# Kernel tuning notes

Hardware: AMD Instinct MI355X
Metric: run time of the kernel (lower is better)

The kernel has to match this reference:

```python
import jax, jax.numpy as jnp
import numpy as np

B, S, D, DI = 8, 4096, 512, 2048
EPS = 1e-12  # torch F.normalize eps


def _l2norm(x):
    n = jnp.sqrt(jnp.sum(x * x, axis=-1, keepdims=True))
    return x / jnp.maximum(n, EPS)


def setup_inputs() -> dict:
    key = jax.random.key(0)
    ks = jax.random.split(key, 10)
    sd = 1.0 / np.sqrt(D)
    si = 1.0 / np.sqrt(DI)
    return {
        "x": jax.random.normal(ks[0], (B, S, D), jnp.float32),
        "wq": jax.random.uniform(ks[1], (D, DI), jnp.float32, -sd, sd),
        "wk": jax.random.uniform(ks[2], (D, DI), jnp.float32, -sd, sd),
        "wv": jax.random.uniform(ks[3], (D, DI), jnp.float32, -sd, sd),
        "wo": jax.random.uniform(ks[4], (DI, D), jnp.float32, -si, si),
        "w1": jax.random.uniform(ks[5], (D, DI), jnp.float32, -sd, sd),
        "b1": jax.random.uniform(ks[6], (DI,), jnp.float32, -sd, sd),
        "w2": jax.random.uniform(ks[7], (DI, D), jnp.float32, -si, si),
        "b2": jax.random.uniform(ks[8], (D,), jnp.float32, -si, si),
    }


def reference(x, wq, wk, wv, wo, w1, b1, w2, b2):
    # Hydra attention (linear): normalize(q) * sum_s(normalize(k)*v)
    q = _l2norm(jnp.einsum('bsd,de->bse', x, wq))
    k = _l2norm(jnp.einsum('bsd,de->bse', x, wk))
    v = jnp.einsum('bsd,de->bse', x, wv)
    kv = jnp.sum(k * v, axis=-2, keepdims=True)  # [B,1,DI]
    attn = jnp.einsum('bse,ed->bsd', q * kv, wo) + x  # dropout = identity (eval)
    # position-wise FFN with residual
    h = jax.nn.relu(jnp.einsum('bsd,de->bse', attn, w1) + b1)
    out = jnp.einsum('bse,ed->bsd', h, w2) + b2 + attn
    return out
```

## Files before the change

### kernel.cpp

```cpp
#include <hip/hip_runtime.h>
#include <stdint.h>

#define Bb  8
#define Ss  4096
#define Dd  512
#define DIi 2048
#define Mm  (Bb*Ss)

typedef unsigned short u16;
typedef __bf16 bf16x8 __attribute__((ext_vector_type(8)));
typedef float  f32x4  __attribute__((ext_vector_type(4)));

__device__ __forceinline__ float bfu(unsigned int u) {
  return __uint_as_float((u & 0xffffu) << 16);
}
__device__ __forceinline__ u16 f2bu(float f) {
  unsigned int x = __float_as_uint(f);
  return (u16)((x + 0x7fffu + ((x >> 16) & 1u)) >> 16);
}

__device__ __forceinline__ void tr_tile(const float* __restrict__ W, u16* __restrict__ Wt,
                                        int K, int N, int local, int tid) {
  __shared__ float t[32][33];
  const int nx = N / 32;
  const int n0 = (local % nx) * 32, k0 = (local / nx) * 32;
  const int tx = tid & 31, ty = tid >> 5;
#pragma unroll
  for (int i = 0; i < 32; i += 8)
    t[ty + i][tx] = W[(long)(k0 + ty + i) * N + n0 + tx];
  __syncthreads();
#pragma unroll
  for (int i = 0; i < 32; i += 8)
    Wt[(long)(n0 + ty + i) * K + k0 + tx] = f2bu(t[tx][ty + i]);
}

__global__ __launch_bounds__(256) void prep(
    const float* __restrict__ x, u16* __restrict__ xb,
    const float* wv, const float* w1, const float* wo, const float* w2,
    const float* wq, const float* wk,
    u16* wvT, u16* w1T, u16* woT, u16* w2T, u16* wqb, u16* wkb,
    float* __restrict__ zptr) {
  const int bid = blockIdx.x, tid = threadIdx.x;
  if (bid < 256) {
    zptr[bid * 256 + tid] = 0.f;
  } else if (bid < 2304) {
    long i = (long)(bid - 256) * 256 + tid;
    const long n4 = (long)Mm * Dd / 4;
    const long st = 2048L * 256;
    for (; i < n4; i += st) {
      float4 v = ((const float4*)x)[i];
      ushort4 o;
      o.x = f2bu(v.x); o.y = f2bu(v.y); o.z = f2bu(v.z); o.w = f2bu(v.w);
      ((ushort4*)xb)[i] = o;
    }
  } else if (bid < 3328)  tr_tile(wv, wvT, Dd, DIi, bid - 2304, tid);
  else if (bid < 4352)    tr_tile(w1, w1T, Dd, DIi, bid - 3328, tid);
  else if (bid < 5376)    tr_tile(wo, woT, DIi, Dd, bid - 4352, tid);
  else if (bid < 6400)    tr_tile(w2, w2T, DIi, Dd, bid - 5376, tid);
  else if (bid < 7424) {
    long i = (long)(bid - 6400) * 256 + tid;
    float4 v = ((const float4*)wq)[i];
    ushort4 o;
    o.x = f2bu(v.x); o.y = f2bu(v.y); o.z = f2bu(v.z); o.w = f2bu(v.w);
    ((ushort4*)wqb)[i] = o;
  } else {
    long i = (long)(bid - 7424) * 256 + tid;
    float4 v = ((const float4*)wk)[i];
    ushort4 o;
    o.x = f2bu(v.x); o.y = f2bu(v.y); o.z = f2bu(v.z); o.w = f2bu(v.w);
    ((ushort4*)wkb)[i] = o;
  }
}

__global__ __launch_bounds__(256) void build_wob(const u16* __restrict__ woT,
                                                 const float* __restrict__ kv,
                                                 u16* __restrict__ wob) {
  const int b = blockIdx.y;
  long i = (long)blockIdx.x * 256 + threadIdx.x;
  const long tot = (long)Dd * DIi / 8;
  if (i >= tot) return;
  const long e = i * 8;
  const int k = (int)(e & (DIi - 1));
  ushort4 w0 = *(const ushort4*)(woT + e);
  ushort4 w1 = *(const ushort4*)(woT + e + 4);
  const float* kvp = kv + (long)b * DIi + k;
  ushort4 o0, o1;
  o0.x = f2bu(bfu(w0.x) * kvp[0]); o0.y = f2bu(bfu(w0.y) * kvp[1]);
  o0.z = f2bu(bfu(w0.z) * kvp[2]); o0.w = f2bu(bfu(w0.w) * kvp[3]);
  o1.x = f2bu(bfu(w1.x) * kvp[4]); o1.y = f2bu(bfu(w1.y) * kvp[5]);
  o1.z = f2bu(bfu(w1.z) * kvp[6]); o1.w = f2bu(bfu(w1.w) * kvp[7]);
  u16* dst = wob + (long)b * Dd * DIi + e;
  *(ushort4*)dst = o0;
  *(ushort4*)(dst + 4) = o1;
}

__global__ void tr_x(const u16* __restrict__ xb, const float* __restrict__ nksq,
                     u16* __restrict__ xT, u16* __restrict__ xrnT) {
  __shared__ u16 t[32][33];
  __shared__ float rns[32];
  const int b = blockIdx.z;
  const int s0 = blockIdx.y * 32, d0 = blockIdx.x * 32;
  const int tx = threadIdx.x, ty = threadIdx.y;
  const size_t sbase = (size_t)b * Ss + s0;
#pragma unroll
  for (int i = 0; i < 32; i += 8)
    t[ty + i][tx] = xb[(sbase + ty + i) * Dd + d0 + tx];
  if (ty == 0) {
    const float nk = fmaxf(nksq[sbase + tx], 0.f);
    rns[tx] = 1.f / fmaxf(sqrtf(nk), 1e-12f);
  }
  __syncthreads();
  const size_t dbase = (size_t)b * Dd + d0;
#pragma unroll
  for (int i = 0; i < 32; i += 8) {
    const u16 v = t[tx][ty + i];
    const size_t idx = (dbase + ty + i) * Ss + s0 + tx;
    xT[idx] = v;
    xrnT[idx] = f2bu(bfu(v) * rns[tx]);
  }
}

__global__ __launch_bounds__(256) void colsum_kv(const u16* __restrict__ wkb,
                                                 const u16* __restrict__ Tb,
                                                 float* __restrict__ kv) {
  const int b = blockIdx.y;
  const int e0 = blockIdx.x * 1024 + threadIdx.x * 4;
  const u16* wp = wkb + e0;
  const u16* tp = Tb + (size_t)b * Dd * DIi + e0;
  float a0 = 0, a1 = 0, a2 = 0, a3 = 0;
  for (int d = 0; d < Dd; ++d) {
    ushort4 w = *(const ushort4*)wp;
    ushort4 t = *(const ushort4*)tp;
    a0 += bfu(w.x) * bfu(t.x);
    a1 += bfu(w.y) * bfu(t.y);
    a2 += bfu(w.z) * bfu(t.z);
    a3 += bfu(w.w) * bfu(t.w);
    wp += DIi; tp += DIi;
  }
  float* o = kv + (size_t)b * DIi + e0;
  o[0] = a0; o[1] = a1; o[2] = a2; o[3] = a3;
}

#define GLL(src, dst) \
  __builtin_amdgcn_global_load_lds((const __attribute__((address_space(1))) unsigned int*)(src), \
                                   (__attribute__((address_space(3))) unsigned int*)(dst), 16, 0, 0)

enum { G_FFN1 = 2, G_FFN2 = 3 };

template<int MODE>
__global__ __launch_bounds__(512, 2) void gemm8(
    const u16* __restrict__ A, const u16* __restrict__ Bt,
    int N, int K,
    u16* __restrict__ Ybf, float* __restrict__ Yf,
    const u16* __restrict__ resb, const float* __restrict__ bias)
{
  __shared__ u16 lds8[65536];

  const int bx = blockIdx.x;
  const int by = blockIdx.y;
  const int tid  = threadIdx.x;
  const int lane = tid & 63;
  const int wid  = tid >> 6;
  const int wr = wid >> 2, wc = wid & 3;
  const int l15 = lane & 15, lg = lane >> 4;

  const long bm0 = (long)by * 256;
  const long bn0 = (long)bx * 256;
  const int NT = K >> 6;

  const u16* pA = A + bm0 * K;
  const u16* pB = Bt + bn0 * K;

  const int rowT = ((tid >> 6) << 3) | (tid & 7);
  const int cc8  = ((tid >> 3) & 7) * 8;

#define STAGE(PTR, LD, H, TT, BUFU, REGU) do {                                  \
    const u16* s0_ = (PTR) + (size_t)((H) * 128 + rowT) * (LD)                  \
                     + (size_t)(TT) * 64 + cc8;                                 \
    u16* d_ = lds8 + (BUFU) + (REGU) + (H) * 8192 + wid * 512;                  \
    GLL(s0_, d_);                                                               \
    GLL(s0_ + (size_t)64 * (LD), d_ + 4096);                                    \
  } while (0)

  const int aoff = (wr * 16384 + (l15 >> 3) * 1024 + lg * 128 + (l15 & 7) * 16) >> 1;
  const int boff = (32768 + (wc >> 1) * 16384 + (wc & 1) * 8192 +
                    (l15 >> 3) * 1024 + lg * 128 + (l15 & 7) * 16) >> 1;
#define LDA(M_, KS_, BU_) (*(const bf16x8*)(lds8 + (BU_) + aoff + (M_) * 1024 + (KS_) * 256))
#define LDB(N_, KS_, BU_) (*(const bf16x8*)(lds8 + (BU_) + boff + (N_) * 1024 + (KS_) * 256))

  f32x4 acc[8][4] = {};

  STAGE(pA, K, 0, 0, 0, 0);
  STAGE(pA, K, 1, 0, 0, 0);
  STAGE(pB, K, 0, 0, 0, 16384);
  STAGE(pB, K, 1, 0, 0, 16384);
  STAGE(pA, K, 0, 1, 32768, 0);
  asm volatile("s_waitcnt vmcnt(2)" ::: "memory");
  __builtin_amdgcn_s_barrier();

  for (int t = 0; t < NT; ++t) {
    const int bufu = (t & 1) * 32768;
    const int nbuf = bufu ^ 32768;
    bf16x8 aF[4], bF[4];

#pragma unroll
    for (int n = 0; n < 4; ++n) bF[n] = LDB(n, 0, bufu);
#pragma unroll
    for (int m = 0; m < 4; ++m) aF[m] = LDA(m, 0, bufu);
    if (t + 1 < NT) STAGE(pA, K, 1, t + 1, nbuf, 0);
    __builtin_amdgcn_s_barrier();
    __builtin_amdgcn_s_setprio(1);
#pragma unroll
    for (int m = 0; m < 4; ++m)
#pragma unroll
      for (int n = 0; n < 4; ++n)
        acc[m][n] = __builtin_amdgcn_mfma_f32_16x16x32_bf16(aF[m], bF[n], acc[m][n], 0, 0, 0);
    __builtin_amdgcn_s_setprio(0);

#pragma unroll
    for (int m = 0; m < 4; ++m) aF[m] = LDA(4 + m, 0, bufu);
    if (t + 1 < NT) STAGE(pB, K, 0, t + 1, nbuf, 16384);
    __builtin_amdgcn_s_barrier();
    __builtin_amdgcn_s_setprio(1);
#pragma unroll
    for (int m = 0; m < 4; ++m)
#pragma unroll
      for (int n = 0; n < 4; ++n)
        acc[4 + m][n] = __builtin_amdgcn_mfma_f32_16x16x32_bf16(aF[m], bF[n], acc[4 + m][n], 0, 0, 0);
    __builtin_amdgcn_s_setprio(0);

#pragma unroll
    for (int n = 0; n < 4; ++n) bF[n] = LDB(n, 1, bufu);
#pragma unroll
    for (int m = 0; m < 4; ++m) aF[m] = LDA(m, 1, bufu);
    if (t + 1 < NT) STAGE(pB, K, 1, t + 1, nbuf, 16384);
    __builtin_amdgcn_s_barrier();
    __builtin_amdgcn_s_setprio(1);
#pragma unroll
    for (int m = 0; m < 4; ++m)
#pragma unroll
      for (int n = 0; n < 4; ++n)
        acc[m][n] = __builtin_amdgcn_mfma_f32_16x16x32_bf16(aF[m], bF[n], acc[m][n], 0, 0, 0);
    __builtin_amdgcn_s_setprio(0);

#pragma unroll
    for (int m = 0; m < 4; ++m) aF[m] = LDA(4 + m, 1, bufu);
    __builtin_amdgcn_s_barrier();
    __builtin_amdgcn_s_setprio(1);
#pragma unroll
    for (int m = 0; m < 4; ++m)
#pragma unroll
      for (int n = 0; n < 4; ++n)
        acc[4 + m][n] = __builtin_amdgcn_mfma_f32_16x16x32_bf16(aF[m], bF[n], acc[4 + m][n], 0, 0, 0);
    __builtin_amdgcn_s_setprio(0);

    if (t + 1 < NT) {
      __builtin_amdgcn_s_barrier();
      if (t + 2 < NT) {
        STAGE(pA, K, 0, t + 2, bufu, 0);
        asm volatile("s_waitcnt vmcnt(2)" ::: "memory");
      } else {
        asm volatile("s_waitcnt vmcnt(0)" ::: "memory");
      }
      __builtin_amdgcn_s_barrier();
    }
  }

#pragma unroll
  for (int m = 0; m < 8; ++m) {
    const long row0 = bm0 + wr * 128 + m * 16 + lg * 4;
#pragma unroll
    for (int n = 0; n < 4; ++n) {
      const long col = bn0 + wc * 64 + n * 16 + l15;
#pragma unroll
      for (int r = 0; r < 4; ++r) {
        const long idx = (row0 + r) * N + col;
        const float v = acc[m][n][r];
        if constexpr (MODE == G_FFN1) {
          float o = v + bias[col];
          o = o > 0.f ? o : 0.f;
          Ybf[idx] = f2bu(o);
        } else {
          Yf[idx] = v + bias[col] + bfu(resb[idx]);
        }
      }
    }
  }
#undef STAGE
#undef LDA
#undef LDB
}

__global__ __launch_bounds__(256) void mega_small(
    const u16* __restrict__ wqb, const u16* __restrict__ wkb,
    const u16* __restrict__ wob,
    u16* __restrict__ Gt, u16* __restrict__ Gkt, u16* __restrict__ Ut, int zbase)
{
  __shared__ u16 As[4096];
  __shared__ u16 Bs[4096];
  const int K = DIi;
  const int idx = blockIdx.z + zbase;
  const u16* A  = (idx == 1) ? wkb : wqb;
  const u16* Bt = (idx == 0) ? wqb : (idx == 1) ? wkb
                  : wob + (size_t)(idx - 2) * Dd * DIi;
  u16* Ct = (idx == 0) ? Gt : (idx == 1) ? Gkt
            : Ut + (size_t)(idx - 2) * Dd * Dd;

  const int tid = threadIdx.x, lane = tid & 63, w = tid >> 6;
  const int wr = w >> 1, wc = w & 1;
  const int l15 = lane & 15, lg = lane >> 4;
  const long bm0 = (long)blockIdx.y * 128;
  const long bn0 = (long)blockIdx.x * 128;

  const int c0 = tid, c1 = tid + 256;
  const u16* aS0 = A  + (bm0 + (c0 >> 2)) * K + (c0 & 3) * 8;
  const u16* aS1 = A  + (bm0 + (c1 >> 2)) * K + (c1 & 3) * 8;
  const u16* bS0 = Bt + (bn0 + (c0 >> 2)) * K + (c0 & 3) * 8;
  const u16* bS1 = Bt + (bn0 + (c1 >> 2)) * K + (c1 & 3) * 8;
  u16* aD0 = As + w * 512;
  u16* aD1 = As + 2048 + w * 512;
  u16* bD0 = Bs + w * 512;
  u16* bD1 = Bs + 2048 + w * 512;

  f32x4 acc[4][4] = {};

  for (int k0 = 0; k0 < K; k0 += 32) {
    GLL(aS0 + k0, aD0);
    GLL(aS1 + k0, aD1);
    GLL(bS0 + k0, bD0);
    GLL(bS1 + k0, bD1);
    __syncthreads();
    bf16x8 af[4], bfv[4];
#pragma unroll
    for (int m = 0; m < 4; ++m)
      af[m] = *(const bf16x8*)(As + (wr * 64 + m * 16 + l15) * 32 + lg * 8);
#pragma unroll
    for (int n = 0; n < 4; ++n)
      bfv[n] = *(const bf16x8*)(Bs + (wc * 64 + n * 16 + l15) * 32 + lg * 8);
#pragma unroll
    for (int m = 0; m < 4; ++m)
#pragma unroll
      for (int n = 0; n < 4; ++n)
        acc[m][n] = __builtin_amdgcn_mfma_f32_16x16x32_bf16(af[m], bfv[n], acc[m][n], 0, 0, 0);
    __syncthreads();
  }

#pragma unroll
  for (int m = 0; m < 4; ++m) {
    const int row0 = (int)bm0 + wr * 64 + m * 16 + lg * 4;
#pragma unroll
    for (int n = 0; n < 4; ++n) {
      const int col = (int)bn0 + wc * 64 + n * 16 + l15;
      ushort4 o;
      o.x = f2bu(acc[m][n][0]); o.y = f2bu(acc[m][n][1]);
      o.z = f2bu(acc[m][n][2]); o.w = f2bu(acc[m][n][3]);
      *(ushort4*)(Ct + (size_t)col * Dd + row0) = o;
    }
  }
}

template<int MODE>
__global__ __launch_bounds__(256) void mega128b(
    const u16* __restrict__ A0, const u16* __restrict__ Bt0,
    u16* __restrict__ C0, int N, int K)
{
  __shared__ u16 As[4096];
  __shared__ u16 Bs[4096];
  const int z = blockIdx.z;
  const u16* A  = A0 + (size_t)z * (MODE == 0 ? (size_t)Dd * Ss : (size_t)Dd * Dd);
  const u16* Bt = (MODE == 0) ? Bt0 + (size_t)z * Dd * Ss : Bt0;
  u16* C = C0 + (size_t)z * (MODE == 0 ? (size_t)Dd * Dd : (size_t)Dd * DIi);

  const int tid = threadIdx.x, lane = tid & 63, w = tid >> 6;
  const int wr = w >> 1, wc = w & 1;
  const int l15 = lane & 15, lg = lane >> 4;
  const long bm0 = (long)blockIdx.y * 128;
  const long bn0 = (long)blockIdx.x * 128;

  const int c0 = tid, c1 = tid + 256;
  const u16* aS0 = A  + (bm0 + (c0 >> 2)) * K + (c0 & 3) * 8;
  const u16* aS1 = A  + (bm0 + (c1 >> 2)) * K + (c1 & 3) * 8;
  const u16* bS0 = Bt + (bn0 + (c0 >> 2)) * K + (c0 & 3) * 8;
  const u16* bS1 = Bt + (bn0 + (c1 >> 2)) * K + (c1 & 3) * 8;
  u16* aD0 = As + w * 512;
  u16* aD1 = As + 2048 + w * 512;
  u16* bD0 = Bs + w * 512;
  u16* bD1 = Bs + 2048 + w * 512;

  f32x4 acc[4][4] = {};

  for (int k0 = 0; k0 < K; k0 += 32) {
    GLL(aS0 + k0, aD0);
    GLL(aS1 + k0, aD1);
    GLL(bS0 + k0, bD0);
    GLL(bS1 + k0, bD1);
    __syncthreads();
    bf16x8 af[4], bfv[4];
#pragma unroll
    for (int m = 0; m < 4; ++m)
      af[m] = *(const bf16x8*)(As + (wr * 64 + m * 16 + l15) * 32 + lg * 8);
#pragma unroll
    for (int n = 0; n < 4; ++n)
      bfv[n] = *(const bf16x8*)(Bs + (wc * 64 + n * 16 + l15) * 32 + lg * 8);
#pragma unroll
    for (int m = 0; m < 4; ++m)
#pragma unroll
      for (int n = 0; n < 4; ++n)
        acc[m][n] = __builtin_amdgcn_mfma_f32_16x16x32_bf16(af[m], bfv[n], acc[m][n], 0, 0, 0);
    __syncthreads();
  }

#pragma unroll
  for (int m = 0; m < 4; ++m) {
    const long row0 = bm0 + wr * 64 + m * 16 + lg * 4;
#pragma unroll
    for (int n = 0; n < 4; ++n) {
      const long col = bn0 + wc * 64 + n * 16 + l15;
#pragma unroll
      for (int r = 0; r < 4; ++r)
        C[(row0 + r) * N + col] = f2bu(acc[m][n][r]);
    }
  }
}

template<int MODE>
__global__ __launch_bounds__(256) void mega_nx(
    const u16* __restrict__ xb, const u16* __restrict__ Gt, const u16* __restrict__ Gkt,
    const u16* __restrict__ Ut,
    float* __restrict__ nqsq, float* __restrict__ nksq, u16* __restrict__ attnb)
{
  __shared__ u16 As[4096];
  __shared__ u16 Bs[4096];
  __shared__ u16 xs[16384];
  const int K = Dd, N = Dd;

  const int tid = threadIdx.x, lane = tid & 63, w = tid >> 6;
  const int wr = w >> 1, wc = w & 1;
  const int l15 = lane & 15, lg = lane >> 4;
  const bool isK = (MODE == 0) && (blockIdx.y >= Mm / 128);
  const long bm0 = (long)(isK ? blockIdx.y - Mm / 128 : blockIdx.y) * 128;
  const long bn0 = (long)blockIdx.x * 128;
  const int bq = (int)(bm0 >> 12);
  const u16* Bt = (MODE == 0) ? (isK ? Gkt : Gt) : Ut + (size_t)bq * Dd * Dd;
  float* nsq = (MODE == 0) ? (isK ? nksq : nqsq) : nqsq;

  const int c0 = tid, c1 = tid + 256;
  const u16* aS0 = xb + (bm0 + (c0 >> 2)) * K + (c0 & 3) * 8;
  const u16* aS1 = xb + (bm0 + (c1 >> 2)) * K + (c1 & 3) * 8;
  const u16* bS0 = Bt + (bn0 + (c0 >> 2)) * K + (c0 & 3) * 8;
  const u16* bS1 = Bt + (bn0 + (c1 >> 2)) * K + (c1 & 3) * 8;
  u16* aD0 = As + w * 512;
  u16* aD1 = As + 2048 + w * 512;
  u16* bD0 = Bs + w * 512;
  u16* bD1 = Bs + 2048 + w * 512;

  f32x4 acc[4][4] = {};

  for (int k0 = 0; k0 < K; k0 += 32) {
    GLL(aS0 + k0, aD0);
    GLL(aS1 + k0, aD1);
    GLL(bS0 + k0, bD0);
    GLL(bS1 + k0, bD1);
    __syncthreads();
    bf16x8 af[4], bfv[4];
#pragma unroll
    for (int m = 0; m < 4; ++m)
      af[m] = *(const bf16x8*)(As + (wr * 64 + m * 16 + l15) * 32 + lg * 8);
#pragma unroll
    for (int n = 0; n < 4; ++n)
      bfv[n] = *(const bf16x8*)(Bs + (wc * 64 + n * 16 + l15) * 32 + lg * 8);
#pragma unroll
    for (int m = 0; m < 4; ++m)
#pragma unroll
      for (int n = 0; n < 4; ++n)
        acc[m][n] = __builtin_amdgcn_mfma_f32_16x16x32_bf16(af[m], bfv[n], acc[m][n], 0, 0, 0);
    __syncthreads();
  }

#pragma unroll
  for (int i = 0; i < 8; ++i) {
    const int c = i * 256 + tid;
    const int rowL = c >> 4;
    const int srcslot = (c & 15) ^ (rowL & 15);
    const u16* src = xb + (size_t)(bm0 + rowL) * Dd + bn0 + srcslot * 8;
    GLL(src, xs + i * 2048 + w * 512);
  }
  asm volatile("s_waitcnt vmcnt(0)" ::: "memory");
  __builtin_amdgcn_s_barrier();

#define XV(RL, CL) bfu(xs[(RL) * 128 + ((((CL) >> 3) ^ ((RL) & 15)) << 3) + ((CL) & 7)])

  if constexpr (MODE == 0) {
    float sk[16];
#pragma unroll
    for (int i = 0; i < 16; ++i) sk[i] = 0.f;
#pragma unroll
    for (int m = 0; m < 4; ++m) {
#pragma unroll
      for (int n = 0; n < 4; ++n) {
        const int colL = wc * 64 + n * 16 + l15;
#pragma unroll
        for (int r = 0; r < 4; ++r) {
          const int rowL = wr * 64 + m * 16 + lg * 4 + r;
          sk[m * 4 + r] += acc[m][n][r] * XV(rowL, colL);
        }
      }
    }
#pragma unroll
    for (int i = 0; i < 16; ++i) {
#pragma unroll
      for (int off = 1; off < 16; off <<= 1)
        sk[i] += __shfl_xor(sk[i], off, 64);
    }
    if (l15 == 0) {
#pragma unroll
      for (int m = 0; m < 4; ++m)
#pragma unroll
        for (int r = 0; r < 4; ++r)
          atomicAdd(&nsq[bm0 + wr * 64 + m * 16 + lg * 4 + r], sk[m * 4 + r]);
    }
  } else {
#pragma unroll
    for (int m = 0; m < 4; ++m) {
      const long row0 = bm0 + wr * 64 + m * 16 + lg * 4;
      float rq[4];
#pragma unroll
      for (int r = 0; r < 4; ++r)
        rq[r] = 1.f / fmaxf(sqrtf(fmaxf(nqsq[row0 + r], 0.f)), 1e-12f);
#pragma unroll
      for (int n = 0; n < 4; ++n) {
        const int colL = wc * 64 + n * 16 + l15;
#pragma unroll
        for (int r = 0; r < 4; ++r) {
          const int rowL = wr * 64 + m * 16 + lg * 4 + r;
          attnb[(row0 + r) * N + bn0 + colL] = f2bu(acc[m][n][r] * rq[r] + XV(rowL, colL));
        }
      }
    }
  }
#undef XV
}

extern "C" void kernel_launch(void* const* d_in, const int* in_sizes, int n_in,
                              void* d_out, int out_size, void* d_ws, size_t ws_size,
                              hipStream_t stream) {
  const float* x  = (const float*)d_in[0];
  const float* wq = (const float*)d_in[1];
  const float* wk = (const float*)d_in[2];
  const float* wv = (const float*)d_in[3];
  const float* wo = (const float*)d_in[4];
  const float* w1 = (const float*)d_in[5];
  const float* b1 = (const float*)d_in[6];
  const float* w2 = (const float*)d_in[7];
  const float* b2 = (const float*)d_in[8];
  float* out = (float*)d_out;

  char* p = (char*)d_ws;
  auto take = [&](size_t bytes) {
    char* r = p; p += (bytes + 255) & ~(size_t)255; return r;
  };
  u16*   xb    = (u16*)take((size_t)Mm * Dd * 2);
  u16*   wvT   = (u16*)take((size_t)DIi * Dd * 2);
  u16*   w1T   = (u16*)take((size_t)DIi * Dd * 2);
  u16*   woT   = (u16*)take((size_t)Dd * DIi * 2);
  u16*   w2T   = (u16*)take((size_t)Dd * DIi * 2);
  u16*   wqb   = (u16*)take((size_t)Dd * DIi * 2);
  u16*   wkb   = (u16*)take((size_t)Dd * DIi * 2);
  u16*   Gt    = (u16*)take((size_t)Dd * Dd * 2);
  u16*   Gkt   = (u16*)take((size_t)Dd * Dd * 2);
  u16*   Ut    = (u16*)take((size_t)Bb * Dd * Dd * 2);
  u16*   buf1  = (u16*)take((size_t)Mm * DIi * 2);
  u16*   attnb = (u16*)take((size_t)Mm * Dd * 2);
  float* nksq  = (float*)take((size_t)Mm * 4);
  float* nqsq  = (float*)take((size_t)Mm * 4);
  float* kvp   = (float*)take((size_t)Bb * DIi * 4);
  u16* xT   = buf1;
  u16* xrnT = buf1 + (size_t)Mm * Dd;
  u16* Tb   = buf1 + 2 * (size_t)Mm * Dd;
  u16* Cb   = buf1 + 2 * (size_t)Mm * Dd + (size_t)Bb * Dd * DIi;
  u16* wob  = buf1 + 2 * (size_t)Mm * Dd + (size_t)Bb * Dd * DIi
                   + (size_t)Bb * Dd * Dd;
  (void)in_sizes; (void)n_in; (void)out_size; (void)ws_size;

  prep<<<8448, 256, 0, stream>>>(x, xb, wv, w1, wo, w2, wq, wk,
                                 wvT, w1T, woT, w2T, wqb, wkb, nksq);

  mega_small<<<dim3(4, 4, 2), 256, 0, stream>>>(wqb, wkb, nullptr, Gt, Gkt, Ut, 0);

  mega_nx<0><<<dim3(4, 2 * Mm / 128), 256, 0, stream>>>(
      xb, Gt, Gkt, nullptr, nqsq, nksq, nullptr);

  tr_x<<<dim3(Dd / 32, Ss / 32, Bb), dim3(32, 8), 0, stream>>>(xb, nksq, xT, xrnT);

  mega128b<0><<<dim3(4, 4, Bb), 256, 0, stream>>>(xrnT, xT, Cb, Dd, Ss);

  mega128b<1><<<dim3(16, 4, Bb), 256, 0, stream>>>(Cb, wvT, Tb, DIi, Dd);

  colsum_kv<<<dim3(2, Bb), 256, 0, stream>>>(wkb, Tb, kvp);

  build_wob<<<dim3(512, Bb), 256, 0, stream>>>(woT, kvp, wob);

  mega_small<<<dim3(4, 4, 8), 256, 0, stream>>>(wqb, wkb, wob, Gt, Gkt, Ut, 2);

  mega_nx<1><<<dim3(4, Mm / 128), 256, 0, stream>>>(
      xb, nullptr, nullptr, Ut, nqsq, nullptr, attnb);

  gemm8<G_FFN1><<<dim3(DIi / 256, Mm / 256), 512, 0, stream>>>(
      attnb, w1T, DIi, Dd, buf1, nullptr, nullptr, b1);

  gemm8<G_FFN2><<<dim3(Dd / 256, Mm / 256), 512, 0, stream>>>(
      buf1, w2T, Dd, DIi, nullptr, out, attnb, b2);
}
```

Baseline: 552.7 us.

## Raise parallelism of the Cb GEMM and split-reduce the kv column sum

The batched xrnT·xT GEMM now uses 64x64 tiles, giving 512 blocks instead of 128, so the long K=4096 reduction is spread over many more CUs. The column-sum kernel that produces kv is split along the D dimension into 8 chunks, and the partial sums are combined with atomicAdd. The prep kernel zeroes a larger region so the kv buffer starts at zero before the atomics. The trade-offs are less data reuse per tile, more global traffic, and atomic contention plus non-deterministic summation order for kv.

```diff
diff --git a/kernel.cpp b/kernel.cpp
--- a/kernel.cpp
+++ b/kernel.cpp
@@ -41,10 +41,10 @@
     u16* wvT, u16* w1T, u16* woT, u16* w2T, u16* wqb, u16* wkb,
     float* __restrict__ zptr) {
   const int bid = blockIdx.x, tid = threadIdx.x;
-  if (bid < 256) {
+  if (bid < 320) {
     zptr[bid * 256 + tid] = 0.f;
-  } else if (bid < 2304) {
-    long i = (long)(bid - 256) * 256 + tid;
+  } else if (bid < 2368) {
+    long i = (long)(bid - 320) * 256 + tid;
     const long n4 = (long)Mm * Dd / 4;
     const long st = 2048L * 256;
     for (; i < n4; i += st) {
@@ -53,18 +53,18 @@
       o.x = f2bu(v.x); o.y = f2bu(v.y); o.z = f2bu(v.z); o.w = f2bu(v.w);
       ((ushort4*)xb)[i] = o;
     }
-  } else if (bid < 3328)  tr_tile(wv, wvT, Dd, DIi, bid - 2304, tid);
-  else if (bid < 4352)    tr_tile(w1, w1T, Dd, DIi, bid - 3328, tid);
-  else if (bid < 5376)    tr_tile(wo, woT, DIi, Dd, bid - 4352, tid);
-  else if (bid < 6400)    tr_tile(w2, w2T, DIi, Dd, bid - 5376, tid);
-  else if (bid < 7424) {
-    long i = (long)(bid - 6400) * 256 + tid;
+  } else if (bid < 3392)  tr_tile(wv, wvT, Dd, DIi, bid - 2368, tid);
+  else if (bid < 4416)    tr_tile(w1, w1T, Dd, DIi, bid - 3392, tid);
+  else if (bid < 5440)    tr_tile(wo, woT, DIi, Dd, bid - 4416, tid);
+  else if (bid < 6464)    tr_tile(w2, w2T, DIi, Dd, bid - 5440, tid);
+  else if (bid < 7488) {
+    long i = (long)(bid - 6464) * 256 + tid;
     float4 v = ((const float4*)wq)[i];
     ushort4 o;
     o.x = f2bu(v.x); o.y = f2bu(v.y); o.z = f2bu(v.z); o.w = f2bu(v.w);
     ((ushort4*)wqb)[i] = o;
   } else {
-    long i = (long)(bid - 7424) * 256 + tid;
+    long i = (long)(bid - 7488) * 256 + tid;
     float4 v = ((const float4*)wk)[i];
     ushort4 o;
     o.x = f2bu(v.x); o.y = f2bu(v.y); o.z = f2bu(v.z); o.w = f2bu(v.w);
@@ -124,21 +124,17 @@
                                                  const u16* __restrict__ Tb,
                                                  float* __restrict__ kv) {
   const int b = blockIdx.y;
-  const int e0 = blockIdx.x * 1024 + threadIdx.x * 4;
-  const u16* wp = wkb + e0;
-  const u16* tp = Tb + (size_t)b * Dd * DIi + e0;
-  float a0 = 0, a1 = 0, a2 = 0, a3 = 0;
-  for (int d = 0; d < Dd; ++d) {
-    ushort4 w = *(const ushort4*)wp;
-    ushort4 t = *(const ushort4*)tp;
-    a0 += bfu(w.x) * bfu(t.x);
-    a1 += bfu(w.y) * bfu(t.y);
-    a2 += bfu(w.z) * bfu(t.z);
-    a3 += bfu(w.w) * bfu(t.w);
+  const int e = blockIdx.x * 256 + threadIdx.x;
+  const int d0 = blockIdx.z * 64;
+  const u16* wp = wkb + (size_t)d0 * DIi + e;
+  const u16* tp = Tb + (size_t)b * Dd * DIi + (size_t)d0 * DIi + e;
+  float a = 0.f;
+#pragma unroll 4
+  for (int d = 0; d < 64; ++d) {
+    a += bfu(wp[0]) * bfu(tp[0]);
     wp += DIi; tp += DIi;
   }
-  float* o = kv + (size_t)b * DIi + e0;
-  o[0] = a0; o[1] = a1; o[2] = a2; o[3] = a3;
+  atomicAdd(&kv[(size_t)b * DIi + e], a);
 }
 
 #define GLL(src, dst) \
@@ -359,17 +355,73 @@
   }
 }
 
-template<int MODE>
-__global__ __launch_bounds__(256) void mega128b(
-    const u16* __restrict__ A0, const u16* __restrict__ Bt0,
-    u16* __restrict__ C0, int N, int K)
+__global__ __launch_bounds__(256) void megacb(
+    const u16* __restrict__ xrnT, const u16* __restrict__ xT,
+    u16* __restrict__ Cb)
+{
+  __shared__ u16 As[2048];
+  __shared__ u16 Bs[2048];
+  const int K = Ss;
+  const int z = blockIdx.z;
+  const u16* A  = xrnT + (size_t)z * Dd * Ss;
+  const u16* Bt = xT   + (size_t)z * Dd * Ss;
+  u16* C = Cb + (size_t)z * Dd * Dd;
+
+  const int tid = threadIdx.x, lane = tid & 63, w = tid >> 6;
+  const int wr = w >> 1, wc = w & 1;
+  const int l15 = lane & 15, lg = lane >> 4;
+  const long bm0 = (long)blockIdx.y * 64;
+  const long bn0 = (long)blockIdx.x * 64;
+
+  const u16* aS0 = A  + (bm0 + (tid >> 2)) * K + (tid & 3) * 8;
+  const u16* bS0 = Bt + (bn0 + (tid >> 2)) * K + (tid & 3) * 8;
+  u16* aD0 = As + w * 512;
+  u16* bD0 = Bs + w * 512;
+
+  f32x4 acc[2][2] = {};
+
+  for (int k0 = 0; k0 < K; k0 += 32) {
+    GLL(aS0 + k0, aD0);
+    GLL(bS0 + k0, bD0);
+    __syncthreads();
+    bf16x8 af[2], bfv[2];
+#pragma unroll
+    for (int m = 0; m < 2; ++m)
+      af[m] = *(const bf16x8*)(As + (wr * 32 + m * 16 + l15) * 32 + lg * 8);
+#pragma unroll
+    for (int n = 0; n < 2; ++n)
+      bfv[n] = *(const bf16x8*)(Bs + (wc * 32 + n * 16 + l15) * 32 + lg * 8);
+#pragma unroll
+    for (int m = 0; m < 2; ++m)
+#pragma unroll
+      for (int n = 0; n < 2; ++n)
+        acc[m][n] = __builtin_amdgcn_mfma_f32_16x16x32_bf16(af[m], bfv[n], acc[m][n], 0, 0, 0);
+    __syncthreads();
+  }
+
+#pragma unroll
+  for (int m = 0; m < 2; ++m) {
+    const long row0 = bm0 + wr * 32 + m * 16 + lg * 4;
+#pragma unroll
+    for (int n = 0; n < 2; ++n) {
+      const long col = bn0 + wc * 32 + n * 16 + l15;
+#pragma unroll
+      for (int r = 0; r < 4; ++r)
+        C[(row0 + r) * Dd + col] = f2bu(acc[m][n][r]);
+    }
+  }
+}
+
+__global__ __launch_bounds__(256) void megatb(
+    const u16* __restrict__ Cb, const u16* __restrict__ wvT,
+    u16* __restrict__ Tb)
 {
   __shared__ u16 As[4096];
   __shared__ u16 Bs[4096];
+  const int K = Dd, N = DIi;
   const int z = blockIdx.z;
-  const u16* A  = A0 + (size_t)z * (MODE == 0 ? (size_t)Dd * Ss : (size_t)Dd * Dd);
-  const u16* Bt = (MODE == 0) ? Bt0 + (size_t)z * Dd * Ss : Bt0;
-  u16* C = C0 + (size_t)z * (MODE == 0 ? (size_t)Dd * Dd : (size_t)Dd * DIi);
+  const u16* A  = Cb + (size_t)z * Dd * Dd;
+  u16* C = Tb + (size_t)z * Dd * DIi;
 
   const int tid = threadIdx.x, lane = tid & 63, w = tid >> 6;
   const int wr = w >> 1, wc = w & 1;
@@ -378,10 +430,10 @@
   const long bn0 = (long)blockIdx.x * 128;
 
   const int c0 = tid, c1 = tid + 256;
-  const u16* aS0 = A  + (bm0 + (c0 >> 2)) * K + (c0 & 3) * 8;
-  const u16* aS1 = A  + (bm0 + (c1 >> 2)) * K + (c1 & 3) * 8;
-  const u16* bS0 = Bt + (bn0 + (c0 >> 2)) * K + (c0 & 3) * 8;
-  const u16* bS1 = Bt + (bn0 + (c1 >> 2)) * K + (c1 & 3) * 8;
+  const u16* aS0 = A   + (bm0 + (c0 >> 2)) * K + (c0 & 3) * 8;
+  const u16* aS1 = A   + (bm0 + (c1 >> 2)) * K + (c1 & 3) * 8;
+  const u16* bS0 = wvT + (bn0 + (c0 >> 2)) * K + (c0 & 3) * 8;
+  const u16* bS1 = wvT + (bn0 + (c1 >> 2)) * K + (c1 & 3) * 8;
   u16* aD0 = As + w * 512;
   u16* aD1 = As + 2048 + w * 512;
   u16* bD0 = Bs + w * 512;
@@ -582,7 +634,7 @@
                    + (size_t)Bb * Dd * Dd;
   (void)in_sizes; (void)n_in; (void)out_size; (void)ws_size;
 
-  prep<<<8448, 256, 0, stream>>>(x, xb, wv, w1, wo, w2, wq, wk,
+  prep<<<8512, 256, 0, stream>>>(x, xb, wv, w1, wo, w2, wq, wk,
                                  wvT, w1T, woT, w2T, wqb, wkb, nksq);
 
   mega_small<<<dim3(4, 4, 2), 256, 0, stream>>>(wqb, wkb, nullptr, Gt, Gkt, Ut, 0);
@@ -592,11 +644,11 @@
 
   tr_x<<<dim3(Dd / 32, Ss / 32, Bb), dim3(32, 8), 0, stream>>>(xb, nksq, xT, xrnT);
 
-  mega128b<0><<<dim3(4, 4, Bb), 256, 0, stream>>>(xrnT, xT, Cb, Dd, Ss);
-
-  mega128b<1><<<dim3(16, 4, Bb), 256, 0, stream>>>(Cb, wvT, Tb, DIi, Dd);
-
-  colsum_kv<<<dim3(2, Bb), 256, 0, stream>>>(wkb, Tb, kvp);
+  megacb<<<dim3(8, 8, Bb), 256, 0, stream>>>(xrnT, xT, Cb);
+
+  megatb<<<dim3(16, 4, Bb), 256, 0, stream>>>(Cb, wvT, Tb);
+
+  colsum_kv<<<dim3(8, Bb, 8), 256, 0, stream>>>(wkb, Tb, kvp);
 
   build_wob<<<dim3(512, Bb), 256, 0, stream>>>(woT, kvp, wob);
 
```

Result: faster. 475.1 us (-14.0%).
